# Performance work log

Measured on AMD Instinct MI355X. Metric: run time of the kernel, lower is better.

The kernel has to match this reference:

```python
import jax, jax.numpy as jnp
import numpy as np

H, W, S, B = 256, 256, 16, 8  # dim=(H,W); S hardcoded in forward; B = 1 + events[-1,-1]
N = 4_000_000


def _shift2d(a, dy, dx):
    """Replicates F.pad(a, (pad(dx) + pad(dy)))[:H,:W] where pad(n)=(n,0) if n>=0 else (0,-n).
    Positive diff shifts content right/down and zero-fills; negative diff is a no-op
    (right/bottom padding followed by top-left crop is identity)."""
    sy = jnp.maximum(dy, 0)
    sx = jnp.maximum(dx, 0)
    a = jnp.roll(a, shift=(sy, sx), axis=(0, 1))
    row = jnp.arange(a.shape[0])[:, None]
    col = jnp.arange(a.shape[1])[None, :]
    return jnp.where((row >= sy) & (col >= sx), a, 0.0)


def setup_inputs():
    key = jax.random.key(0)
    k1, k2, k3, k4 = jax.random.split(key, 4)
    x = jax.random.randint(k1, (N,), 0, W).astype(jnp.float32)
    y = jax.random.randint(k2, (N,), 0, H).astype(jnp.float32)
    t = jax.random.uniform(k3, (N,), minval=1e-3, maxval=1.0)
    p = (jax.random.randint(k4, (N,), 0, 2) * 2 - 1).astype(jnp.float32)
    b = jnp.repeat(jnp.arange(B, dtype=jnp.float32), N // B)  # sorted so events[-1,-1]==B-1
    events = jnp.stack([x, y, t, p, b], axis=1)
    return {"events": events}


def _forward(events):
    x = events[:, 0]
    y = events[:, 1]
    t = events[:, 2]
    bi = events[:, 4].astype(jnp.int32)

    # per-batch time normalization: t /= max(t) within each sample
    t_max = jax.ops.segment_max(t, bi, num_segments=B)
    t = t / t_max[bi]

    xi = x.astype(jnp.int32)
    yi = y.astype(jnp.int32)

    # container: per-pixel event count histogram, (B,H,W)
    idx_c = xi + W * yi + W * H * bi
    container = jnp.zeros(B * H * W, jnp.int32).at[idx_c].add(1).reshape(B, H, W)

    # time_segment[e] = number of thresholds i/S (i=1..S-1) with t >= i/S
    thr = jnp.arange(1, S, dtype=t.dtype) / S
    ts = jnp.searchsorted(thr, t, side='right').astype(jnp.int32)

    # combiner accumulates the segment index itself (as in the torch code)
    idx_cb = xi + W * yi + W * H * ts + W * H * S * bi
    combiner = jnp.zeros(B * S * H * W, jnp.int32).at[idx_cb].add(ts)
    combiner = combiner.reshape(B, S, H, W).astype(jnp.float32)

    # per-(batch, segment) event counts and x/y centroids
    seg = bi * S + ts
    cnt = jax.ops.segment_sum(jnp.ones_like(t), seg, num_segments=B * S).reshape(B, S)
    xm = jax.ops.segment_sum(x, seg, num_segments=B * S).reshape(B, S) / cnt
    ym = jax.ops.segment_sum(y, seg, num_segments=B * S).reshape(B, S) / cnt

    # mean-shift alignment + accumulation of the S segment images
    combined = []
    for b_ in range(B):
        segment = combiner[b_, 0]
        x_mean = xm[b_, 0]
        y_mean = ym[b_, 0]
        pts = cnt[b_, 0]  # note: never updated in the original code
        for i in range(1, S):
            cond = cnt[b_, i] > pts
            tmp = jnp.where(cond, segment, combiner[b_, i])
            base = jnp.where(cond, combiner[b_, i], segment)
            dx = jnp.floor(jnp.where(cond, xm[b_, i] - x_mean, x_mean - xm[b_, i])).astype(jnp.int32)
            dy = jnp.floor(jnp.where(cond, ym[b_, i] - y_mean, y_mean - ym[b_, i])).astype(jnp.int32)
            x_mean = jnp.where(cond, xm[b_, i], x_mean)
            y_mean = jnp.where(cond, ym[b_, i], y_mean)
            segment = base + _shift2d(tmp, dy, dx)
        combined.append(jax.nn.relu(segment - S))
    combined_img = jnp.stack(combined)  # (B,H,W)

    # half-resolution count + mean-timestamp voxel grids
    hw4 = (H // 2) * (W // 2)
    idx_ct = xi // 2 + (W // 2) * (yi // 2) + (W * H * bi) // 4
    counter = jnp.zeros(B * hw4, jnp.int32).at[idx_ct].add(1).astype(jnp.float32)
    divider = jnp.where(counter == 0, 1.0, counter)
    timer = jnp.zeros(B * hw4, jnp.float32).at[idx_ct].add(t) / divider
    counter = counter.reshape(B, H // 2, W // 2)
    timer = timer.reshape(B, H // 2, W // 2)

    # 2x2 difference pooling of the count image
    dyv = container[:, ::2] - container[:, 1::2]
    dyv = (dyv[:, :, ::2] + dyv[:, :, 1::2]).astype(jnp.float32)
    dxv = container[:, :, ::2] - container[:, :, 1::2]
    dxv = (dxv[:, 1::2] + dxv[:, ::2]).astype(jnp.float32)

    # F.interpolate(scale_factor=0.5, mode='nearest') == ::2 subsampling for even H,W
    combined_half = combined_img[:, ::2, ::2]

    return jnp.stack([dxv, dyv, timer, counter, combined_half], axis=1)  # (B,5,H/2,W/2)


def reference(events):
    return _forward(events)
```

## Files before the change

kernel.cpp:

```cpp
#include <hip/hip_runtime.h>

#define SS 16
#define BB 8
#define CHUNKS 32

#define OFF_CNT    0
#define OFF_XS     512
#define OFF_YS     1024
#define OFF_TMAX   1536
#define OFF_P4REP  2048
#define OFF_CMREP  (2048 + 33554432)
#define ZERO_BYTES 1568


__global__ void k_tmax(const float4* __restrict__ ev4, int nq, unsigned* __restrict__ tmax) {
    int bb = blockIdx.x >> 7;
    long base = (long)bb * nq;
    unsigned m = 0;
    for (int q = (blockIdx.x & 127) * blockDim.x + threadIdx.x; q < nq; q += 128 * blockDim.x) {
        const float4* p = ev4 + (base + q) * 5;
        float4 f0 = p[0], f1 = p[1], f3 = p[3], f4 = p[4];
        unsigned t0 = __float_as_uint(f0.z), t1 = __float_as_uint(f1.w);
        unsigned t2 = __float_as_uint(f3.x), t3 = __float_as_uint(f4.y);
        unsigned a = t0 > t1 ? t0 : t1;
        unsigned b = t2 > t3 ? t2 : t3;
        a = a > b ? a : b;
        m = m > a ? m : a;
    }
    __shared__ unsigned sm;
    if (threadIdx.x == 0) sm = 0;
    __syncthreads();
    atomicMax(&sm, m);
    __syncthreads();
    if (threadIdx.x == 0) atomicMax(&tmax[bb], sm);
}

__global__ void __launch_bounds__(1024, 1)
k_main(const float4* __restrict__ ev4, int nq,
       const unsigned* __restrict__ tmax,
       unsigned long long* __restrict__ p4rep,
       int* __restrict__ cnt, int* __restrict__ xs, int* __restrict__ ys) {
    __shared__ unsigned long long p4s[16384];
    __shared__ unsigned long long stat[SS];
    int bb = blockIdx.x >> 5;
    int ch = blockIdx.x & 31;
    for (int i = threadIdx.x; i < 16384; i += 1024) p4s[i] = 0ull;
    if (threadIdx.x < SS) stat[threadIdx.x] = 0ull;
    __syncthreads();
    float tm = __uint_as_float(tmax[bb]);
    long base = (long)bb * nq;
    for (int q = ch * 1024 + threadIdx.x; q < nq; q += CHUNKS * 1024) {
        const float4* p = ev4 + (base + q) * 5;
        float4 f0 = p[0], f1 = p[1], f2 = p[2], f3 = p[3], f4 = p[4];
        float X[4] = { f0.x, f1.y, f2.z, f3.w };
        float Y[4] = { f0.y, f1.z, f2.w, f4.x };
        float T[4] = { f0.z, f1.w, f3.x, f4.y };
        #pragma unroll
        for (int k = 0; k < 4; k++) {
            int xi = (int)X[k], yi = (int)Y[k];
            float tn = __fdiv_rn(T[k], tm);
            int ts = (int)(tn * 16.0f);
            if (ts > 15) ts = 15;
            unsigned qfix = __float2uint_rn(tn * 262144.0f);
            unsigned long long v = (unsigned long long)qfix
                | (1ull << 28)
                | ((unsigned long long)((xi & 1) ^ 1) << 40)
                | ((unsigned long long)((yi & 1) ^ 1) << 52);
            atomicAdd(&p4s[((yi >> 1) << 7) + (xi >> 1)], v);
            atomicAdd(&stat[ts], 1ull | ((unsigned long long)xi << 20)
                                      | ((unsigned long long)yi << 42));
        }
    }
    __syncthreads();
    unsigned long long* dst = p4rep + (long)blockIdx.x * 16384;
    for (int i = threadIdx.x; i < 16384; i += 1024) dst[i] = p4s[i];
    if (threadIdx.x < SS) {
        unsigned long long v = stat[threadIdx.x];
        if (v) {
            int g = bb * SS + threadIdx.x;
            atomicAdd(&cnt[g], (int)(v & 0xFFFFF));
            atomicAdd(&xs[g],  (int)((v >> 20) & 0x3FFFFF));
            atomicAdd(&ys[g],  (int)(v >> 42));
        }
    }
}

__global__ void __launch_bounds__(1024, 1)
k_comb(const float4* __restrict__ ev4, int nq,
       const unsigned* __restrict__ tmax,
       const int* __restrict__ cnt, const int* __restrict__ xs, const int* __restrict__ ys,
       int* __restrict__ cmrep) {
    __shared__ int combs[16384];
    __shared__ double xm[SS], ym[SS];
    __shared__ int cs[SS], ssy[SS], ssx[SS];
    int bb = blockIdx.x >> 5;
    int ch = blockIdx.x & 31;
    for (int i = threadIdx.x; i < 16384; i += 1024) combs[i] = 0;
    if (threadIdx.x < SS) {
        int g = bb * SS + threadIdx.x;
        int cc = cnt[g];
        cs[threadIdx.x] = cc;
        xm[threadIdx.x] = (double)xs[g] / (double)cc;
        ym[threadIdx.x] = (double)ys[g] / (double)cc;
    }
    __syncthreads();
    if (threadIdx.x == 0) {
        double x_mean = xm[0], y_mean = ym[0];
        int c0 = cs[0];
        int sy[SS], sx[SS];
        for (int k = 0; k < SS; k++) { sy[k] = 0; sx[k] = 0; }
        for (int k = 1; k < SS; k++) {
            bool cond = cs[k] > c0;
            double ddx = cond ? (xm[k] - x_mean) : (x_mean - xm[k]);
            double ddy = cond ? (ym[k] - y_mean) : (y_mean - ym[k]);
            int dx = (int)floor(ddx);
            int dy = (int)floor(ddy);
            int px = dx > 0 ? dx : 0;
            int py = dy > 0 ? dy : 0;
            if (cond) {
                for (int j = 0; j < k; j++) { sy[j] += py; sx[j] += px; }
                x_mean = xm[k]; y_mean = ym[k];
            } else {
                sy[k] = py; sx[k] = px;
            }
        }
        for (int k = 0; k < SS; k++) { ssy[k] = sy[k]; ssx[k] = sx[k]; }
    }
    __syncthreads();
    float tm = __uint_as_float(tmax[bb]);
    long base = (long)bb * nq;
    for (int q = ch * 1024 + threadIdx.x; q < nq; q += CHUNKS * 1024) {
        const float4* p = ev4 + (base + q) * 5;
        float4 f0 = p[0], f1 = p[1], f2 = p[2], f3 = p[3], f4 = p[4];
        float X[4] = { f0.x, f1.y, f2.z, f3.w };
        float Y[4] = { f0.y, f1.z, f2.w, f4.x };
        float T[4] = { f0.z, f1.w, f3.x, f4.y };
        #pragma unroll
        for (int k = 0; k < 4; k++) {
            int xi = (int)X[k], yi = (int)Y[k];
            float tn = __fdiv_rn(T[k], tm);
            int ts = (int)(tn * 16.0f);
            if (ts > 15) ts = 15;
            if (ts) {
                int yy = yi + ssy[ts];
                int xx = xi + ssx[ts];
                if (yy < 256 && xx < 256 && !((yy | xx) & 1))
                    atomicAdd(&combs[((yy >> 1) << 7) + (xx >> 1)], ts);
            }
        }
    }
    __syncthreads();
    int* dst = cmrep + (long)blockIdx.x * 16384;
    for (int i = threadIdx.x; i < 16384; i += 1024) dst[i] = combs[i];
}

__global__ void k_out(const unsigned long long* __restrict__ p4rep,
                      const int* __restrict__ cmrep, float* __restrict__ out) {
    int lin = blockIdx.x * blockDim.x + threadIdx.x;
    int hp = lin & 16383;
    int b  = lin >> 14;
    long rb = (long)b * CHUNKS * 16384 + hp;
    unsigned tfix = 0; int c = 0, Ex = 0, Ey = 0, cm = 0;
    #pragma unroll 8
    for (int r = 0; r < CHUNKS; r++) {
        unsigned long long v = p4rep[rb + (long)r * 16384];
        tfix += (unsigned)(v & 0xFFFFFFFull);
        c    += (int)((v >> 28) & 0xFFF);
        Ex   += (int)((v >> 40) & 0xFFF);
        Ey   += (int)((v >> 52) & 0xFFF);
        cm   += cmrep[rb + (long)r * 16384];
    }
    float tsum = (float)(double)tfix * (1.0f / 262144.0f);
    float dxv = (float)(2 * Ex - c);
    float dyv = (float)(2 * Ey - c);
    float ctr = (float)c;
    float tmr = tsum / (c == 0 ? 1.0f : ctr);
    float cmb = (float)cm - 16.0f;
    cmb = cmb < 0.0f ? 0.0f : cmb;
    int obase = (b * 5) << 14;
    out[obase              + hp] = dxv;
    out[obase +     16384  + hp] = dyv;
    out[obase + 2 * 16384  + hp] = tmr;
    out[obase + 3 * 16384  + hp] = ctr;
    out[obase + 4 * 16384  + hp] = cmb;
}

extern "C" void kernel_launch(void* const* d_in, const int* in_sizes, int n_in,
                              void* d_out, int out_size, void* d_ws, size_t ws_size,
                              hipStream_t stream) {
    const float4* ev4 = (const float4*)d_in[0];
    int n  = in_sizes[0] / 5;
    int nb = n / BB;
    int nq = nb / 4;
    char* ws = (char*)d_ws;
    int*      cnt  = (int*)     (ws + OFF_CNT);
    int*      xs   = (int*)     (ws + OFF_XS);
    int*      ys   = (int*)     (ws + OFF_YS);
    unsigned* tmax = (unsigned*)(ws + OFF_TMAX);
    unsigned long long* p4rep = (unsigned long long*)(ws + OFF_P4REP);
    int*      cmrep = (int*)    (ws + OFF_CMREP);

    hipMemsetAsync(d_ws, 0, ZERO_BYTES, stream);
    hipLaunchKernelGGL(k_tmax, dim3(1024), dim3(256),  0, stream, ev4, nq, tmax);
    hipLaunchKernelGGL(k_main, dim3(256),  dim3(1024), 0, stream, ev4, nq, tmax,
                       p4rep, cnt, xs, ys);
    hipLaunchKernelGGL(k_comb, dim3(256),  dim3(1024), 0, stream, ev4, nq, tmax,
                       cnt, xs, ys, cmrep);
    hipLaunchKernelGGL(k_out,  dim3(512),  dim3(256),  0, stream, p4rep, cmrep,
                       (float*)d_out);
}
```

Measured before the change: 160.7 us.

## Fuse all stages into one cooperative kernel and cache per-event records for combiner pass

```diff
diff --git a/kernel.cpp b/kernel.cpp
--- a/kernel.cpp
+++ b/kernel.cpp
@@ -1,4 +1,7 @@
 #include <hip/hip_runtime.h>
+#include <hip/hip_cooperative_groups.h>
+
+namespace cg = cooperative_groups;
 
 #define SS 16
 #define BB 8
@@ -10,51 +13,64 @@
 #define OFF_TMAX   1536
 #define OFF_P4REP  2048
 #define OFF_CMREP  (2048 + 33554432)
-#define ZERO_BYTES 1568
-
-
-__global__ void k_tmax(const float4* __restrict__ ev4, int nq, unsigned* __restrict__ tmax) {
-    int bb = blockIdx.x >> 7;
-    long base = (long)bb * nq;
+#define OFF_REC    (2048 + 33554432 + 16777216)
+
+
+__global__ void __launch_bounds__(1024, 1)
+k_fused(const float4* __restrict__ ev4, int nq,
+        unsigned* __restrict__ tmax,
+        int* __restrict__ cnt, int* __restrict__ xs, int* __restrict__ ys,
+        unsigned long long* __restrict__ p4rep, int* __restrict__ cmrep,
+        uint4* __restrict__ rec4, float* __restrict__ out) {
+    cg::grid_group grid = cg::this_grid();
+    __shared__ unsigned long long p4s[16384];
+    __shared__ unsigned long long stat[SS];
+    __shared__ double xm[SS], ym[SS];
+    __shared__ int cs[SS], ssy[SS], ssx[SS];
+    __shared__ unsigned smax;
+
+    const int bb = blockIdx.x >> 5;
+    const int ch = blockIdx.x & 31;
+    const int tid = threadIdx.x;
+    const long base = (long)bb * nq;
+
+    if (tid < BB * SS) { cnt[tid] = 0; xs[tid] = 0; ys[tid] = 0; }
+    if (tid < BB) tmax[tid] = 0u;
+    if (tid == 0) smax = 0u;
+    grid.sync();
+
     unsigned m = 0;
-    for (int q = (blockIdx.x & 127) * blockDim.x + threadIdx.x; q < nq; q += 128 * blockDim.x) {
+    for (int q = ch * 1024 + tid; q < nq; q += CHUNKS * 1024) {
         const float4* p = ev4 + (base + q) * 5;
         float4 f0 = p[0], f1 = p[1], f3 = p[3], f4 = p[4];
         unsigned t0 = __float_as_uint(f0.z), t1 = __float_as_uint(f1.w);
         unsigned t2 = __float_as_uint(f3.x), t3 = __float_as_uint(f4.y);
         unsigned a = t0 > t1 ? t0 : t1;
-        unsigned b = t2 > t3 ? t2 : t3;
-        a = a > b ? a : b;
+        unsigned b2 = t2 > t3 ? t2 : t3;
+        a = a > b2 ? a : b2;
         m = m > a ? m : a;
     }
-    __shared__ unsigned sm;
-    if (threadIdx.x == 0) sm = 0;
-    __syncthreads();
-    atomicMax(&sm, m);
-    __syncthreads();
-    if (threadIdx.x == 0) atomicMax(&tmax[bb], sm);
-}
-
-__global__ void __launch_bounds__(1024, 1)
-k_main(const float4* __restrict__ ev4, int nq,
-       const unsigned* __restrict__ tmax,
-       unsigned long long* __restrict__ p4rep,
-       int* __restrict__ cnt, int* __restrict__ xs, int* __restrict__ ys) {
-    __shared__ unsigned long long p4s[16384];
-    __shared__ unsigned long long stat[SS];
-    int bb = blockIdx.x >> 5;
-    int ch = blockIdx.x & 31;
-    for (int i = threadIdx.x; i < 16384; i += 1024) p4s[i] = 0ull;
-    if (threadIdx.x < SS) stat[threadIdx.x] = 0ull;
-    __syncthreads();
-    float tm = __uint_as_float(tmax[bb]);
-    long base = (long)bb * nq;
-    for (int q = ch * 1024 + threadIdx.x; q < nq; q += CHUNKS * 1024) {
+    #pragma unroll
+    for (int off = 32; off; off >>= 1) {
+        unsigned o = (unsigned)__shfl_xor((int)m, off, 64);
+        m = m > o ? m : o;
+    }
+    if ((tid & 63) == 0 && m) atomicMax(&smax, m);
+    __syncthreads();
+    if (tid == 0 && smax) atomicMax(&tmax[bb], smax);
+    grid.sync();
+
+    for (int i = tid; i < 16384; i += 1024) p4s[i] = 0ull;
+    if (tid < SS) stat[tid] = 0ull;
+    __syncthreads();
+    const float tm = __uint_as_float(tmax[bb]);
+    for (int q = ch * 1024 + tid; q < nq; q += CHUNKS * 1024) {
         const float4* p = ev4 + (base + q) * 5;
         float4 f0 = p[0], f1 = p[1], f2 = p[2], f3 = p[3], f4 = p[4];
         float X[4] = { f0.x, f1.y, f2.z, f3.w };
         float Y[4] = { f0.y, f1.z, f2.w, f4.x };
         float T[4] = { f0.z, f1.w, f3.x, f4.y };
+        unsigned r[4];
         #pragma unroll
         for (int k = 0; k < 4; k++) {
             int xi = (int)X[k], yi = (int)Y[k];
@@ -69,42 +85,36 @@
             atomicAdd(&p4s[((yi >> 1) << 7) + (xi >> 1)], v);
             atomicAdd(&stat[ts], 1ull | ((unsigned long long)xi << 20)
                                       | ((unsigned long long)yi << 42));
-        }
-    }
-    __syncthreads();
-    unsigned long long* dst = p4rep + (long)blockIdx.x * 16384;
-    for (int i = threadIdx.x; i < 16384; i += 1024) dst[i] = p4s[i];
-    if (threadIdx.x < SS) {
-        unsigned long long v = stat[threadIdx.x];
+            r[k] = (unsigned)xi | ((unsigned)yi << 8) | ((unsigned)ts << 16);
+        }
+        rec4[base + q] = make_uint4(r[0], r[1], r[2], r[3]);
+    }
+    __syncthreads();
+    {
+        unsigned long long* dst = p4rep + (long)blockIdx.x * 16384;
+        for (int i = tid; i < 16384; i += 1024) dst[i] = p4s[i];
+    }
+    if (tid < SS) {
+        unsigned long long v = stat[tid];
         if (v) {
-            int g = bb * SS + threadIdx.x;
+            int g = bb * SS + tid;
             atomicAdd(&cnt[g], (int)(v & 0xFFFFF));
             atomicAdd(&xs[g],  (int)((v >> 20) & 0x3FFFFF));
             atomicAdd(&ys[g],  (int)(v >> 42));
         }
     }
-}
-
-__global__ void __launch_bounds__(1024, 1)
-k_comb(const float4* __restrict__ ev4, int nq,
-       const unsigned* __restrict__ tmax,
-       const int* __restrict__ cnt, const int* __restrict__ xs, const int* __restrict__ ys,
-       int* __restrict__ cmrep) {
-    __shared__ int combs[16384];
-    __shared__ double xm[SS], ym[SS];
-    __shared__ int cs[SS], ssy[SS], ssx[SS];
-    int bb = blockIdx.x >> 5;
-    int ch = blockIdx.x & 31;
-    for (int i = threadIdx.x; i < 16384; i += 1024) combs[i] = 0;
-    if (threadIdx.x < SS) {
-        int g = bb * SS + threadIdx.x;
+    __threadfence();
+    grid.sync();
+
+    if (tid < SS) {
+        int g = bb * SS + tid;
         int cc = cnt[g];
-        cs[threadIdx.x] = cc;
-        xm[threadIdx.x] = (double)xs[g] / (double)cc;
-        ym[threadIdx.x] = (double)ys[g] / (double)cc;
-    }
-    __syncthreads();
-    if (threadIdx.x == 0) {
+        cs[tid] = cc;
+        xm[tid] = (double)xs[g] / (double)cc;
+        ym[tid] = (double)ys[g] / (double)cc;
+    }
+    __syncthreads();
+    if (tid == 0) {
         double x_mean = xm[0], y_mean = ym[0];
         int c0 = cs[0];
         int sy[SS], sx[SS];
@@ -126,63 +136,61 @@
         }
         for (int k = 0; k < SS; k++) { ssy[k] = sy[k]; ssx[k] = sx[k]; }
     }
-    __syncthreads();
-    float tm = __uint_as_float(tmax[bb]);
-    long base = (long)bb * nq;
-    for (int q = ch * 1024 + threadIdx.x; q < nq; q += CHUNKS * 1024) {
-        const float4* p = ev4 + (base + q) * 5;
-        float4 f0 = p[0], f1 = p[1], f2 = p[2], f3 = p[3], f4 = p[4];
-        float X[4] = { f0.x, f1.y, f2.z, f3.w };
-        float Y[4] = { f0.y, f1.z, f2.w, f4.x };
-        float T[4] = { f0.z, f1.w, f3.x, f4.y };
+    int* combs = (int*)p4s;
+    for (int i = tid; i < 16384; i += 1024) combs[i] = 0;
+    __syncthreads();
+    for (int q = ch * 1024 + tid; q < nq; q += CHUNKS * 1024) {
+        uint4 rv = rec4[base + q];
+        unsigned R[4] = { rv.x, rv.y, rv.z, rv.w };
         #pragma unroll
         for (int k = 0; k < 4; k++) {
-            int xi = (int)X[k], yi = (int)Y[k];
-            float tn = __fdiv_rn(T[k], tm);
-            int ts = (int)(tn * 16.0f);
-            if (ts > 15) ts = 15;
+            unsigned r = R[k];
+            int ts = r >> 16;
             if (ts) {
-                int yy = yi + ssy[ts];
-                int xx = xi + ssx[ts];
+                int yy = ((r >> 8) & 255) + ssy[ts];
+                int xx = (r & 255) + ssx[ts];
                 if (yy < 256 && xx < 256 && !((yy | xx) & 1))
                     atomicAdd(&combs[((yy >> 1) << 7) + (xx >> 1)], ts);
             }
         }
     }
     __syncthreads();
-    int* dst = cmrep + (long)blockIdx.x * 16384;
-    for (int i = threadIdx.x; i < 16384; i += 1024) dst[i] = combs[i];
-}
-
-__global__ void k_out(const unsigned long long* __restrict__ p4rep,
-                      const int* __restrict__ cmrep, float* __restrict__ out) {
-    int lin = blockIdx.x * blockDim.x + threadIdx.x;
-    int hp = lin & 16383;
-    int b  = lin >> 14;
-    long rb = (long)b * CHUNKS * 16384 + hp;
-    unsigned tfix = 0; int c = 0, Ex = 0, Ey = 0, cm = 0;
-    #pragma unroll 8
-    for (int r = 0; r < CHUNKS; r++) {
-        unsigned long long v = p4rep[rb + (long)r * 16384];
-        tfix += (unsigned)(v & 0xFFFFFFFull);
-        c    += (int)((v >> 28) & 0xFFF);
-        Ex   += (int)((v >> 40) & 0xFFF);
-        Ey   += (int)((v >> 52) & 0xFFF);
-        cm   += cmrep[rb + (long)r * 16384];
-    }
-    float tsum = (float)(double)tfix * (1.0f / 262144.0f);
-    float dxv = (float)(2 * Ex - c);
-    float dyv = (float)(2 * Ey - c);
-    float ctr = (float)c;
-    float tmr = tsum / (c == 0 ? 1.0f : ctr);
-    float cmb = (float)cm - 16.0f;
-    cmb = cmb < 0.0f ? 0.0f : cmb;
-    int obase = (b * 5) << 14;
-    out[obase              + hp] = dxv;
-    out[obase +     16384  + hp] = dyv;
-    out[obase + 2 * 16384  + hp] = tmr;
-    out[obase + 3 * 16384  + hp] = ctr;
-    out[obase + 4 * 16384  + hp] = cmb;
+    {
+        int* dst = cmrep + (long)blockIdx.x * 16384;
+        for (int i = tid; i < 16384; i += 1024) dst[i] = combs[i];
+    }
+    __threadfence();
+    grid.sync();
+
+    if (tid < 512) {
+        int lin = blockIdx.x * 512 + tid;
+        int hp = lin & 16383;
+        int b  = lin >> 14;
+        long rb = (long)b * CHUNKS * 16384 + hp;
+        unsigned tfix = 0; int c = 0, Ex = 0, Ey = 0, cm = 0;
+        #pragma unroll 8
+        for (int r = 0; r < CHUNKS; r++) {
+            unsigned long long v = p4rep[rb + (long)r * 16384];
+            tfix += (unsigned)(v & 0xFFFFFFFull);
+            c    += (int)((v >> 28) & 0xFFF);
+            Ex   += (int)((v >> 40) & 0xFFF);
+            Ey   += (int)((v >> 52) & 0xFFF);
+            cm   += cmrep[rb + (long)r * 16384];
+        }
+        float tsum = (float)(double)tfix * (1.0f / 262144.0f);
+        float dxv = (float)(2 * Ex - c);
+        float dyv = (float)(2 * Ey - c);
+        float ctr = (float)c;
+        float tmr = tsum / (c == 0 ? 1.0f : ctr);
+        float cmb = (float)cm - 16.0f;
+        cmb = cmb < 0.0f ? 0.0f : cmb;
+        int obase = (b * 5) << 14;
+        out[obase              + hp] = dxv;
+        out[obase +     16384  + hp] = dyv;
+        out[obase + 2 * 16384  + hp] = tmr;
+        out[obase + 3 * 16384  + hp] = ctr;
+        out[obase + 4 * 16384  + hp] = cmb;
+    }
 }
 
 extern "C" void kernel_launch(void* const* d_in, const int* in_sizes, int n_in,
@@ -199,13 +207,11 @@
     unsigned* tmax = (unsigned*)(ws + OFF_TMAX);
     unsigned long long* p4rep = (unsigned long long*)(ws + OFF_P4REP);
     int*      cmrep = (int*)    (ws + OFF_CMREP);
-
-    hipMemsetAsync(d_ws, 0, ZERO_BYTES, stream);
-    hipLaunchKernelGGL(k_tmax, dim3(1024), dim3(256),  0, stream, ev4, nq, tmax);
-    hipLaunchKernelGGL(k_main, dim3(256),  dim3(1024), 0, stream, ev4, nq, tmax,
-                       p4rep, cnt, xs, ys);
-    hipLaunchKernelGGL(k_comb, dim3(256),  dim3(1024), 0, stream, ev4, nq, tmax,
-                       cnt, xs, ys, cmrep);
-    hipLaunchKernelGGL(k_out,  dim3(512),  dim3(256),  0, stream, p4rep, cmrep,
-                       (float*)d_out);
+    uint4*    rec4  = (uint4*)  (ws + OFF_REC);
+    float*    outp  = (float*)d_out;
+
+    void* args[] = { (void*)&ev4, (void*)&nq, (void*)&tmax,
+                     (void*)&cnt, (void*)&xs, (void*)&ys,
+                     (void*)&p4rep, (void*)&cmrep, (void*)&rec4, (void*)&outp };
+    hipLaunchCooperativeKernel((void*)k_fused, dim3(256), dim3(1024), args, 0, stream);
 }
```

Result: slower. 484.1 us (+201.3%).
